# Performance work log

Hardware: AMD Instinct MI355X
Metric: run time of the kernel (lower is better)

Reference implementation:

```python
import jax, jax.numpy as jnp
import numpy as np

N_AGENTS = 32768
FEAT_DIM = 64    # input_dim
N_FRAMES = 64
SEG_SIZE = 8     # agents per scene -> 4096 segments


def setup_inputs() -> dict:
    key = jax.random.key(0)
    in_features = jax.random.normal(key, (N_AGENTS, FEAT_DIM, N_FRAMES), dtype=jnp.float32)
    starts = jnp.arange(0, N_AGENTS, SEG_SIZE, dtype=jnp.int32)
    ends = starts + SEG_SIZE
    seq_start_end = jnp.stack([starts, ends], axis=1)  # [4096, 2], contiguous partition of [0, N)
    return {"in_features": in_features, "seq_start_end": seq_start_end}


def reference(in_features, seq_start_end):
    # Torch module: per segment, permute to [T, n_i, D], mean over D, repeat D times,
    # cat over segments, permute back -> out[n, d, t] = mean_{d'} in[n, d', t].
    # The segment loop is a no-op on the math (mean is per-agent); seq_start_end
    # only defines the (order-preserving) concat, so we compute it in one fused pass.
    mean_feat = jnp.mean(in_features, axis=1, keepdims=True)      # [N, 1, T]
    return jnp.broadcast_to(mean_feat, in_features.shape)          # [N, D, T]
```

## Files before the change

kernel.cpp:

```cpp
#include <hip/hip_runtime.h>

#define N_AGENTS 32768
#define FEAT_DIM 64
#define N_FRAMES 64

__global__ __launch_bounds__(256) void mean_bcast_kernel(const float4* __restrict__ in4,
                                                         float4* __restrict__ out4) {
    const int gid = blockIdx.x * blockDim.x + threadIdx.x;
    const int n   = gid >> 4;
    const int cg  = gid & 15;
    const size_t base = (size_t)n * (FEAT_DIM * N_FRAMES / 4) + cg;

    float4 acc = make_float4(0.f, 0.f, 0.f, 0.f);
    #pragma unroll 16
    for (int d = 0; d < FEAT_DIM; ++d) {
        float4 v = in4[base + (size_t)d * (N_FRAMES / 4)];
        acc.x += v.x;
        acc.y += v.y;
        acc.z += v.z;
        acc.w += v.w;
    }

    const float s = 1.0f / (float)FEAT_DIM;
    const float4 m = make_float4(acc.x * s, acc.y * s, acc.z * s, acc.w * s);

    #pragma unroll 16
    for (int d = 0; d < FEAT_DIM; ++d) {
        out4[base + (size_t)d * (N_FRAMES / 4)] = m;
    }
}

extern "C" void kernel_launch(void* const* d_in, const int* in_sizes, int n_in,
                              void* d_out, int out_size, void* d_ws, size_t ws_size,
                              hipStream_t stream) {
    (void)in_sizes; (void)n_in; (void)d_ws; (void)ws_size; (void)out_size;
    const float4* in4 = (const float4*)d_in[0];
    float4* out4      = (float4*)d_out;

    const int total_threads = N_AGENTS * (N_FRAMES / 4);
    const int block = 256;
    const int grid  = total_threads / block;
    mean_bcast_kernel<<<grid, block, 0, stream>>>(in4, out4);
}
```

Before: 833.3 us.

## Assign one wavefront per agent with shuffle reduction and nontemporal accesses

The work is remapped so that each 64-lane wavefront handles one agent instead of 16 threads per agent. Each lane issues 16 independent float4 loads, the partial sums across feature rows are combined with xor shuffles, and the mean is written back with nontemporal stores. The goal is more memory-level parallelism and more threads in flight on a bandwidth-bound kernel (about 1 GiB of traffic). In exchange it adds shuffle reductions, and the nontemporal hints change caching behaviour.

```diff
diff --git a/kernel.cpp b/kernel.cpp
--- a/kernel.cpp
+++ b/kernel.cpp
@@ -4,41 +4,48 @@
 #define FEAT_DIM 64
 #define N_FRAMES 64
 
-__global__ __launch_bounds__(256) void mean_bcast_kernel(const float4* __restrict__ in4,
-                                                         float4* __restrict__ out4) {
-    const int gid = blockIdx.x * blockDim.x + threadIdx.x;
-    const int n   = gid >> 4;
-    const int cg  = gid & 15;
-    const size_t base = (size_t)n * (FEAT_DIM * N_FRAMES / 4) + cg;
+typedef float v4f __attribute__((ext_vector_type(4)));
 
-    float4 acc = make_float4(0.f, 0.f, 0.f, 0.f);
-    #pragma unroll 16
-    for (int d = 0; d < FEAT_DIM; ++d) {
-        float4 v = in4[base + (size_t)d * (N_FRAMES / 4)];
-        acc.x += v.x;
-        acc.y += v.y;
-        acc.z += v.z;
-        acc.w += v.w;
+__global__ __launch_bounds__(256) void mean_bcast_wave(const v4f* __restrict__ in4,
+                                                       v4f* __restrict__ out4) {
+    const int gtid = blockIdx.x * blockDim.x + threadIdx.x;
+    const int agent = gtid >> 6;
+    const int lane  = threadIdx.x & 63;
+    const size_t base = (size_t)agent * (FEAT_DIM * N_FRAMES / 4) + lane;
+
+    v4f v[16];
+    #pragma unroll
+    for (int c = 0; c < 16; ++c)
+        v[c] = __builtin_nontemporal_load(&in4[base + c * 64]);
+
+    v4f acc = v[0];
+    #pragma unroll
+    for (int c = 1; c < 16; ++c)
+        acc += v[c];
+
+    #pragma unroll
+    for (int i = 0; i < 4; ++i) {
+        float t = acc[i];
+        t += __shfl_xor(t, 16);
+        t += __shfl_xor(t, 32);
+        acc[i] = t;
     }
+    acc *= (1.0f / (float)FEAT_DIM);
 
-    const float s = 1.0f / (float)FEAT_DIM;
-    const float4 m = make_float4(acc.x * s, acc.y * s, acc.z * s, acc.w * s);
-
-    #pragma unroll 16
-    for (int d = 0; d < FEAT_DIM; ++d) {
-        out4[base + (size_t)d * (N_FRAMES / 4)] = m;
-    }
+    #pragma unroll
+    for (int c = 0; c < 16; ++c)
+        __builtin_nontemporal_store(acc, &out4[base + c * 64]);
 }
 
 extern "C" void kernel_launch(void* const* d_in, const int* in_sizes, int n_in,
                               void* d_out, int out_size, void* d_ws, size_t ws_size,
                               hipStream_t stream) {
     (void)in_sizes; (void)n_in; (void)d_ws; (void)ws_size; (void)out_size;
-    const float4* in4 = (const float4*)d_in[0];
-    float4* out4      = (float4*)d_out;
+    const v4f* in4 = (const v4f*)d_in[0];
+    v4f* out4      = (v4f*)d_out;
 
-    const int total_threads = N_AGENTS * (N_FRAMES / 4);
+    const int total_threads = N_AGENTS * 64;
     const int block = 256;
     const int grid  = total_threads / block;
-    mean_bcast_kernel<<<grid, block, 0, stream>>>(in4, out4);
+    mean_bcast_wave<<<grid, block, 0, stream>>>(in4, out4);
 }
```

Result: no change. 838.3 us (+0.6%).
